# Kernel optimization log

Measured on AMD Instinct MI355X. Metric: run time of the kernel, lower is better.

## Reference

```python
import jax, jax.numpy as jnp
import numpy as np

NCA_HIDDEN = 16
N_CODES = 32
EMBED_DIM = 64


def conv2d(x, w, pad, b=None):
    # x: (N, Cin, H, W), w: (Cout, Cin, kh, kw)
    y = jax.lax.conv_general_dilated(
        x, w, window_strides=(1, 1), padding=[(pad, pad), (pad, pad)],
        dimension_numbers=('NCHW', 'OIHW', 'NCHW'))
    if b is not None:
        y = y + b[None, :, None, None]
    return y


def setup_inputs() -> dict:
    key = jax.random.key(0)
    ks = jax.random.split(key, 32)
    rn = lambda k, shp, s=0.05: jax.random.normal(k, shp, dtype=jnp.float32) * s
    H = NCA_HIDDEN
    upd = H * H * 3 * 3  # 2304
    tau = H * H          # 256
    inp = {
        'demo_inputs':  jax.random.normal(ks[0], (8, 1, 64, 64), dtype=jnp.float32),
        'demo_outputs': jax.random.normal(ks[1], (8, 1, 64, 64), dtype=jnp.float32),
        'test_input':   jax.random.normal(ks[2], (16, 1, 256, 256), dtype=jnp.float32),
        # TaskEncoder params
        'enc_w1': rn(ks[3], (16, 2, 3, 3)),  'enc_b1': jnp.zeros((16,), jnp.float32),
        'enc_w2': rn(ks[4], (32, 16, 3, 3)), 'enc_b2': jnp.zeros((32,), jnp.float32),
        'enc_lw': rn(ks[5], (EMBED_DIM, 32)), 'enc_lb': jnp.zeros((EMBED_DIM,), jnp.float32),
        # gen_update hypernet
        'gu_w1': rn(ks[6], (128, EMBED_DIM)), 'gu_b1': jnp.zeros((128,), jnp.float32),
        'gu_w2': rn(ks[7], (upd, 128)),       'gu_b2': jnp.zeros((upd,), jnp.float32),
        # gen_tau hypernet
        'gt_w1': rn(ks[8], (64, EMBED_DIM)),  'gt_b1': jnp.zeros((64,), jnp.float32),
        'gt_w2': rn(ks[9], (tau, 64)),        'gt_b2': jnp.zeros((tau,), jnp.float32),
        # stem
        'stem_w': rn(ks[10], (H, 1, 3, 3)), 'stem_b': jnp.zeros((H,), jnp.float32),
        # VQ codebook, init U(-1/n_codes, 1/n_codes)
        'codebook': jax.random.uniform(ks[11], (N_CODES, H), jnp.float32,
                                       minval=-1.0 / N_CODES, maxval=1.0 / N_CODES),
        # decoder 1x1 conv
        'dec_w': rn(ks[12], (1, H, 1, 1)), 'dec_b': jnp.zeros((1,), jnp.float32),
        'n_steps': 5,
    }
    return inp


def reference(demo_inputs, demo_outputs, test_input,
              enc_w1, enc_b1, enc_w2, enc_b2, enc_lw, enc_lb,
              gu_w1, gu_b1, gu_w2, gu_b2,
              gt_w1, gt_b1, gt_w2, gt_b2,
              stem_w, stem_b, codebook, dec_w, dec_b, n_steps):
    H = NCA_HIDDEN
    # --- Task encoder: mean task embedding over demo pairs ---
    pairs = jnp.concatenate([demo_inputs, demo_outputs], axis=1)  # (N,2,h,w)
    h = jax.nn.relu(conv2d(pairs, enc_w1, 1, enc_b1))
    h = jax.nn.relu(conv2d(h, enc_w2, 1, enc_b2))
    h = h.mean(axis=(2, 3))                   # AdaptiveAvgPool2d(1)+Flatten -> (N,32)
    te = (h @ enc_lw.T + enc_lb).mean(axis=0)  # (embed_dim,)
    # --- Hypernetworks generate NCA weights ---
    W_update = (jax.nn.relu(te @ gu_w1.T + gu_b1) @ gu_w2.T + gu_b2).reshape(H, H, 3, 3)
    W_tau = (jax.nn.relu(te @ gt_w1.T + gt_b1) @ gt_w2.T + gt_b2).reshape(H, H, 1, 1)
    # --- Stem ---
    state = jax.nn.relu(conv2d(test_input, stem_w, 1, stem_b))  # (B,16,Hh,Ww)
    cb_sq = (codebook ** 2).sum(axis=1)  # (n_codes,)
    for _ in range(int(n_steps)):
        delta = jax.nn.relu(conv2d(state, W_update, 1))
        beta = jax.nn.sigmoid(conv2d(state, W_tau, 0))
        state = beta * state + (1.0 - beta) * delta
        # --- VQ step (straight-through) ---
        B, C, Hh, Ww = state.shape
        zf = state.transpose(0, 2, 3, 1).reshape(-1, C)  # (B*Hh*Ww, C)
        dists = (zf ** 2).sum(1, keepdims=True) + cb_sq - 2.0 * (zf @ codebook.T)
        idx = jnp.argmin(dists, axis=1)
        zq = codebook[idx].reshape(B, Hh, Ww, C).transpose(0, 3, 1, 2)
        state = state + jax.lax.stop_gradient(zq - state)
    output = jax.nn.sigmoid(conv2d(state, dec_w, 0, dec_b))
    return output
```

## Files before the change

kernel.cpp:

```cpp
#include <hip/hip_runtime.h>
#include <stdint.h>

#define NPIX 65536
#define NIMG 16

typedef float4 F4;
typedef _Float16 h2v __attribute__((ext_vector_type(2)));
typedef _Float16 h8v __attribute__((ext_vector_type(8)));
typedef float    f4v __attribute__((ext_vector_type(4)));

union H8 { h8v v; h2v p[4]; _Float16 e[8]; };

__device__ __forceinline__ float sigm(float x){ return 1.0f/(1.0f+__expf(-x)); }

#if defined(__has_builtin)
#if __has_builtin(__builtin_amdgcn_rcpf)
#define FRCP(x) __builtin_amdgcn_rcpf(x)
#endif
#endif
#ifndef FRCP
#define FRCP(x) (1.0f/(x))
#endif
__device__ __forceinline__ float sigmf(float x){ return FRCP(1.0f + __expf(-x)); }

__device__ __forceinline__ h2v pkrtz(float a, float b){
  return __builtin_bit_cast(h2v, __builtin_amdgcn_cvt_pkrtz(a,b));
}

#if defined(__has_builtin)
#if __has_builtin(__builtin_amdgcn_fdot2)
#define FDOT2(a,b,c) __builtin_amdgcn_fdot2((a),(b),(c),false)
#endif
#endif
#ifndef FDOT2
#define FDOT2(a,b,c) ((c) + (float)(a)[0]*(float)(b)[0] + (float)(a)[1]*(float)(b)[1])
#endif

__global__ __launch_bounds__(256) void k_enc1(
    const float* __restrict__ din, const float* __restrict__ dou,
    const float* __restrict__ w1, const float* __restrict__ b1,
    float* __restrict__ h1)
{
  int n = blockIdx.x;
  int p = blockIdx.y*256 + threadIdx.x;
  int y = p >> 6, x = p & 63;
  const float* in0 = din + n*4096;
  const float* in1 = dou + n*4096;
  float acc[16];
  #pragma unroll
  for(int c=0;c<16;c++) acc[c]=b1[c];
  for(int ky=0;ky<3;ky++){
    int yy=y+ky-1; if((unsigned)yy>=64u) continue;
    for(int kx=0;kx<3;kx++){
      int xx=x+kx-1; if((unsigned)xx>=64u) continue;
      float v0=in0[yy*64+xx], v1=in1[yy*64+xx];
      #pragma unroll
      for(int co=0;co<16;co++)
        acc[co] += w1[co*18+ky*3+kx]*v0 + w1[co*18+9+ky*3+kx]*v1;
    }
  }
  F4* o=(F4*)(h1 + (size_t)(n*4096+p)*16);
  o[0]=make_float4(fmaxf(acc[0],0.f),fmaxf(acc[1],0.f),fmaxf(acc[2],0.f),fmaxf(acc[3],0.f));
  o[1]=make_float4(fmaxf(acc[4],0.f),fmaxf(acc[5],0.f),fmaxf(acc[6],0.f),fmaxf(acc[7],0.f));
  o[2]=make_float4(fmaxf(acc[8],0.f),fmaxf(acc[9],0.f),fmaxf(acc[10],0.f),fmaxf(acc[11],0.f));
  o[3]=make_float4(fmaxf(acc[12],0.f),fmaxf(acc[13],0.f),fmaxf(acc[14],0.f),fmaxf(acc[15],0.f));
}

__global__ __launch_bounds__(256) void k_enc2(
    const float* __restrict__ h1, const float* __restrict__ w2,
    const float* __restrict__ b2, float* __restrict__ pooled)
{
  int n = blockIdx.x;
  int p = blockIdx.y*256 + threadIdx.x;
  int y = p >> 6, x = p & 63;
  float acc[32];
  #pragma unroll
  for(int c=0;c<32;c++) acc[c]=b2[c];
  for(int ky=0;ky<3;ky++){
    int yy=y+ky-1; if((unsigned)yy>=64u) continue;
    for(int kx=0;kx<3;kx++){
      int xx=x+kx-1; if((unsigned)xx>=64u) continue;
      const F4* hp=(const F4*)(h1 + (size_t)(n*4096 + yy*64+xx)*16);
      F4 a0=hp[0],a1=hp[1],a2=hp[2],a3=hp[3];
      float hv[16]={a0.x,a0.y,a0.z,a0.w,a1.x,a1.y,a1.z,a1.w,
                    a2.x,a2.y,a2.z,a2.w,a3.x,a3.y,a3.z,a3.w};
      #pragma unroll
      for(int ci=0;ci<16;ci++){
        float v=hv[ci];
        #pragma unroll
        for(int co=0;co<32;co++)
          acc[co] = fmaf(w2[co*144 + ci*9 + ky*3+kx], v, acc[co]);
      }
    }
  }
  #pragma unroll
  for(int c=0;c<32;c++) acc[c]=fmaxf(acc[c],0.f);
  __shared__ float red[4][32];
  int lane = threadIdx.x & 63, wv = threadIdx.x >> 6;
  #pragma unroll
  for(int c=0;c<32;c++){
    float v=acc[c];
    for(int off=32;off>=1;off>>=1) v += __shfl_down(v, off, 64);
    if(lane==0) red[wv][c]=v;
  }
  __syncthreads();
  if(threadIdx.x<32){
    float s = red[0][threadIdx.x]+red[1][threadIdx.x]+red[2][threadIdx.x]+red[3][threadIdx.x];
    atomicAdd(&pooled[n*32+threadIdx.x], s);
  }
}

__global__ __launch_bounds__(256) void k_hyperA(
    const float* __restrict__ pooled,
    const float* __restrict__ lw, const float* __restrict__ lb,
    const float* __restrict__ guw1, const float* __restrict__ gub1,
    const float* __restrict__ gtw1, const float* __restrict__ gtb1,
    const float* __restrict__ gtw2, const float* __restrict__ gtb2,
    const float* __restrict__ cb, const float* __restrict__ decw, const float* __restrict__ decb,
    float* __restrict__ hid_g,
    _Float16* __restrict__ wfrag_g,
    _Float16* __restrict__ Mh_g,
    _Float16* __restrict__ bcb_g, _Float16* __restrict__ omb_g,
    _Float16* __restrict__ cbh_g,
    float* __restrict__ chs_g, float* __restrict__ dvals_g)
{
  __shared__ float hm[32], te_s[64], hid_s[128], hidt_s[64];
  __shared__ float wt_s[256];
  __shared__ float cb_s[512];
  int t = threadIdx.x;
  for(int i=t;i<2560;i+=256) ((unsigned int*)wfrag_g)[i]=0u;
  for(int i=t;i<2508;i+=256) ((unsigned int*)Mh_g)[i]=0u;
  if(t<32){
    float s=0.f;
    for(int n=0;n<8;n++) s += pooled[n*32+t];
    hm[t] = s * (1.0f/32768.0f);
  }
  for(int i=t;i<512;i+=256) cb_s[i]=cb[i];
  __syncthreads();
  if(t<64){
    float s=lb[t];
    for(int c=0;c<32;c++) s = fmaf(lw[t*32+c], hm[c], s);
    te_s[t]=s;
  }
  __syncthreads();
  if(t<128){
    float s=gub1[t];
    for(int j=0;j<64;j++) s = fmaf(guw1[t*64+j], te_s[j], s);
    s=fmaxf(s,0.f);
    hid_s[t]=s; hid_g[t]=s;
  } else if(t<192){
    int i=t-128;
    float s=gtb1[i];
    for(int j=0;j<64;j++) s = fmaf(gtw1[i*64+j], te_s[j], s);
    hidt_s[i]=fmaxf(s,0.f);
  }
  __syncthreads();
  {
    float s=gtb2[t];
    for(int i=0;i<64;i++) s = fmaf(gtw2[t*64+i], hidt_s[i], s);
    int co=t>>4, ci=t&15;
    wt_s[ci*16+co]=s;
  }
  __syncthreads();
  {
    int ci=t>>4, co=t&15;
    int g=ci>>3, j=ci&7, lane=(g<<4)|co;
    wfrag_g[(448+lane)*8+j]=(_Float16)wt_s[ci*16+co];
  }
  for(int o=t;o<512;o+=256){
    int k=o>>4, c=o&15;
    float T=0.f;
    for(int ci=0;ci<16;ci++) T = fmaf(wt_s[ci*16+c], cb_s[k*16+ci], T);
    float beta=sigm(T);
    bcb_g[o]=(_Float16)(beta*cb_s[o]);
    omb_g[o]=(_Float16)(1.f-beta);
    cbh_g[o]=(_Float16)cb_s[o];
  }
  if(t<32){
    float sq=0.f, d=0.f;
    for(int c=0;c<16;c++){ float v=cb_s[t*16+c]; sq=fmaf(v,v,sq); d=fmaf(decw[c],v,d); }
    chs_g[t]=0.5f*sq;
    dvals_g[t]=sigm(d+decb[0]);
  }
}

__global__ __launch_bounds__(256) void k_hyperB(
    const float* __restrict__ guw2, const float* __restrict__ gub2,
    const float* __restrict__ hid_g, const float* __restrict__ cb,
    _Float16* __restrict__ wfrag_g, _Float16* __restrict__ Mh_g)
{
  __shared__ float hid_s[128];
  __shared__ float wu_s[256];
  __shared__ float cb_s[512];
  const int t=threadIdx.x, tp=blockIdx.x;
  if(t<128) hid_s[t]=hid_g[t];
  for(int i=t;i<512;i+=256) cb_s[i]=cb[i];
  __syncthreads();
  const int ci=t>>4, co=t&15;
  const int o=co*144+ci*9+tp;
  float s=gub2[o];
  const F4* gp=(const F4*)(guw2+(size_t)o*128);
  #pragma unroll
  for(int i=0;i<32;i++){
    F4 g=gp[i];
    s=fmaf(g.x,hid_s[4*i],s); s=fmaf(g.y,hid_s[4*i+1],s);
    s=fmaf(g.z,hid_s[4*i+2],s); s=fmaf(g.w,hid_s[4*i+3],s);
  }
  wu_s[ci*16+co]=s;
  {
    int k=tp*16+ci;
    int ks=k>>5, rem=k&31, g2=rem>>3, j=rem&7, lane=(g2<<4)|co;
    wfrag_g[(ks*64+lane)*8+j]=(_Float16)s;
  }
  __syncthreads();
  for(int o2=t;o2<512;o2+=256){
    int k=o2>>4, c=o2&15;
    float m=0.f;
    for(int c2=0;c2<16;c2++) m=fmaf(wu_s[c2*16+c], cb_s[k*16+c2], m);
    Mh_g[k*152+tp*16+c]=(_Float16)m;
  }
}

#define ST_STRIDE 3
struct S1P1 { h8v st[324*ST_STRIDE]; float in[400]; };
union S1U { S1P1 p; unsigned int dt[256*20]; };

__global__ __launch_bounds__(256) void k_step1(
    const float* __restrict__ tin,
    const float* __restrict__ stw, const float* __restrict__ stb,
    const _Float16* __restrict__ wfrag,
    const _Float16* __restrict__ cbh, const float* __restrict__ chs,
    uint8_t* __restrict__ idx_out)
{
  __shared__ S1U u;
  __shared__ h8v cb8_s[64];
  __shared__ float chs_s[32];
  __shared__ h2v stwp_s[72];
  __shared__ h2v stbp_s[8];

  const int tid=threadIdx.x;
  const int bx=blockIdx.x, by=blockIdx.y, n=blockIdx.z;
  const float* in = tin + (size_t)n*NPIX;

  for(int i=tid;i<400;i+=256){
    int sy=i/20, sx=i-sy*20;
    int gy=by*16-2+sy, gx=bx*16-2+sx;
    u.p.in[i] = ((unsigned)gy<256u && (unsigned)gx<256u) ? in[gy*256+gx] : 0.0f;
  }
  if(tid<72){
    int q=tid/9, tp=tid-q*9;
    stwp_s[q*9+tp]=pkrtz(stw[(2*q)*9+tp], stw[(2*q+1)*9+tp]);
  } else if(tid<80){
    int q=tid-72;
    stbp_s[q]=pkrtz(stb[2*q], stb[2*q+1]);
  } else if(tid>=160 && tid<192) chs_s[tid-160]=chs[tid-160];
  if(tid<64) ((uint4*)cb8_s)[tid] = ((const uint4*)cbh)[tid];

  const int lane = tid & 63, w = tid >> 6;
  const int g = lane >> 4, nn = lane & 15;
  h8v Bd[5], Bt2;
  const h8v* wf = (const h8v*)wfrag;
  #pragma unroll
  for(int ks=0;ks<5;ks++) Bd[ks]=wf[ks*64+lane];
  Bt2 = wf[7*64+lane];

  __syncthreads();

  for(int p=tid;p<324;p+=256){
    int syh=p/18, sxh=p-syh*18;
    int gy=by*16-1+syh, gx=bx*16-1+sxh;
    H8 b0,b1;
    if((unsigned)gy<256u && (unsigned)gx<256u){
      h2v a2[8];
      #pragma unroll
      for(int q=0;q<8;q++) a2[q]=stbp_s[q];
      #pragma unroll
      for(int ky=0;ky<3;ky++){
        #pragma unroll
        for(int kx=0;kx<3;kx++){
          int tp=ky*3+kx;
          float v=u.p.in[(syh+ky)*20+(sxh+kx)];
          h2v vv=pkrtz(v,v);
          #pragma unroll
          for(int q=0;q<8;q++) a2[q] = stwp_s[q*9+tp]*vv + a2[q];
        }
      }
      b0.p[0]=a2[0]; b0.p[1]=a2[1]; b0.p[2]=a2[2]; b0.p[3]=a2[3];
      b1.p[0]=a2[4]; b1.p[1]=a2[5]; b1.p[2]=a2[6]; b1.p[3]=a2[7];
      #pragma unroll
      for(int c=0;c<8;c++){
        b0.e[c]=b0.e[c]>(_Float16)0?b0.e[c]:(_Float16)0;
        b1.e[c]=b1.e[c]>(_Float16)0?b1.e[c]:(_Float16)0;
      }
    } else {
      b0.v=(h8v){0,0,0,0,0,0,0,0};
      b1.v=(h8v){0,0,0,0,0,0,0,0};
    }
    u.p.st[p*ST_STRIDE]  =b0.v;
    u.p.st[p*ST_STRIDE+1]=b1.v;
  }
  __syncthreads();

  f4v accd[4], acct[4];
  #pragma unroll
  for(int m=0;m<4;m++){ accd[m]=(f4v){0.f,0.f,0.f,0.f}; acct[m]=(f4v){0.f,0.f,0.f,0.f}; }
  #pragma unroll
  for(int ks=0;ks<5;ks++){
    int t = 2*ks + (g>>1); if(t>8) t=8;
    int tyo=(t*11)>>5, txo=t-tyo*3;
    int sel = g&1;
    #pragma unroll
    for(int m=0;m<4;m++){
      int sy = 4*w+m+tyo;
      h8v a = u.p.st[(sy*18 + nn + txo)*ST_STRIDE + sel];
      accd[m]=__builtin_amdgcn_mfma_f32_16x16x32_f16(a,Bd[ks],accd[m],0,0,0);
      if(ks==2) acct[m]=__builtin_amdgcn_mfma_f32_16x16x32_f16(a,Bt2,acct[m],0,0,0);
    }
  }
  const int py=tid>>4, pxx=tid&15;
  const int cpx=((py+1)*18+pxx+1)*ST_STRIDE;
  h8v z0=u.p.st[cpx], z1=u.p.st[cpx+1];
  __syncthreads();

  #pragma unroll
  for(int m=0;m<4;m++){
    #pragma unroll
    for(int r=0;r<4;r++){
      int px=(4*w+m)*16 + g*4 + r;
      h2v pk = pkrtz(accd[m][r], acct[m][r]);
      u.dt[px*20+nn] = __builtin_bit_cast(unsigned int, pk);
    }
  }
  __syncthreads();

  const uint4* dr=(const uint4*)(u.dt+tid*20);
  uint4 q0=dr[0],q1=dr[1],q2=dr[2],q3=dr[3];
  unsigned int qq[16]={q0.x,q0.y,q0.z,q0.w,q1.x,q1.y,q1.z,q1.w,
                       q2.x,q2.y,q2.z,q2.w,q3.x,q3.y,q3.z,q3.w};
  float zn[16];
  #pragma unroll
  for(int c=0;c<16;c++){
    h2v dt2=__builtin_bit_cast(h2v, qq[c]);
    float d=(float)dt2[0]; d = d>0.f?d:0.f;
    float beta=sigmf((float)dt2[1]);
    float zv = (c<8)? (float)z0[c] : (float)z1[c-8];
    zn[c]=fmaf(beta, zv-d, d);
  }
  H8 u0,u1;
  #pragma unroll
  for(int j=0;j<4;j++){
    u0.p[j]=pkrtz(zn[2*j],zn[2*j+1]);
    u1.p[j]=pkrtz(zn[8+2*j],zn[9+2*j]);
  }
  int best=0; float bv=-3.4e38f;
  #pragma unroll
  for(int k=0;k<32;k++){
    H8 c0,c1; c0.v=cb8_s[k*2]; c1.v=cb8_s[k*2+1];
    float dot=0.f;
    #pragma unroll
    for(int j=0;j<4;j++) dot=FDOT2(u0.p[j],c0.p[j],dot);
    #pragma unroll
    for(int j=0;j<4;j++) dot=FDOT2(u1.p[j],c1.p[j],dot);
    float val=dot-chs_s[k];
    if(val>bv){bv=val;best=k;}
  }
  idx_out[(size_t)n*NPIX + (by*16+py)*256 + (bx*16+pxx)]=(uint8_t)best;
}

__global__ __launch_bounds__(256) void k_stepN(
    const uint8_t* __restrict__ idx_in,
    const uint4* __restrict__ Mh,
    const _Float16* __restrict__ bcbh, const _Float16* __restrict__ ombh,
    const _Float16* __restrict__ cbh,  const float* __restrict__ chs,
    const float* __restrict__ dvals,
    uint8_t* __restrict__ idx_out, float* __restrict__ out, int last)
{
  __shared__ int id_s[324];
  __shared__ uint4 M_s[627];
  __shared__ h8v bcb_s[64], omb_s[64], cb8_s[64];
  __shared__ float chs_s[32], dv_s[32];
  const int tid=threadIdx.x;
  const int bx=blockIdx.x, by=blockIdx.y, n=blockIdx.z;
  const uint8_t* ip = idx_in + (size_t)n*NPIX;

  for(int i=tid;i<324;i+=256){
    int sy=i/18, sx=i-sy*18;
    int gy=by*16-1+sy, gx=bx*16-1+sx;
    id_s[i] = ((unsigned)gy<256u && (unsigned)gx<256u) ? (int)ip[gy*256+gx] : 32;
  }
  for(int i=tid;i<627;i+=256) M_s[i]=Mh[i];
  if(tid<64)        ((uint4*)bcb_s)[tid]     = ((const uint4*)bcbh)[tid];
  else if(tid<128)  ((uint4*)omb_s)[tid-64]  = ((const uint4*)ombh)[tid-64];
  else if(tid<192)  ((uint4*)cb8_s)[tid-128] = ((const uint4*)cbh)[tid-128];
  else if(tid<224)  chs_s[tid-192]=chs[tid-192];
  else              dv_s[tid-224]=dvals[tid-224];
  __syncthreads();

  const int py=tid>>4, pxx=tid&15;
  int ida[9];
  #pragma unroll
  for(int dy=0;dy<3;dy++)
    #pragma unroll
    for(int dx=0;dx<3;dx++)
      ida[dy*3+dx]=id_s[(py+dy)*18+pxx+dx];

  const h8v* Mv=(const h8v*)M_s;
  h8v a0={0,0,0,0,0,0,0,0}, a1={0,0,0,0,0,0,0,0};
  #pragma unroll
  for(int t=0;t<9;t++){
    const h8v* mp=&Mv[ida[t]*19+t*2];
    a0+=mp[0]; a1+=mp[1];
  }
  int kc=ida[4];
  h8v r0,r1;
  #pragma unroll
  for(int q=0;q<8;q++){
    r0[q]=a0[q]>(_Float16)0?a0[q]:(_Float16)0;
    r1[q]=a1[q]>(_Float16)0?a1[q]:(_Float16)0;
  }
  H8 u0,u1;
  u0.v = bcb_s[kc*2]   + omb_s[kc*2]  *r0;
  u1.v = bcb_s[kc*2+1] + omb_s[kc*2+1]*r1;
  int best=0; float bv=-3.4e38f;
  #pragma unroll
  for(int k=0;k<32;k++){
    H8 c0,c1; c0.v=cb8_s[k*2]; c1.v=cb8_s[k*2+1];
    float dot=0.f;
    #pragma unroll
    for(int j=0;j<4;j++) dot=FDOT2(u0.p[j],c0.p[j],dot);
    #pragma unroll
    for(int j=0;j<4;j++) dot=FDOT2(u1.p[j],c1.p[j],dot);
    float val=dot-chs_s[k];
    if(val>bv){bv=val;best=k;}
  }
  size_t gidx=(size_t)n*NPIX + (size_t)(by*16+py)*256 + bx*16+pxx;
  if(last) out[gidx]=dv_s[best];
  else     idx_out[gidx]=(uint8_t)best;
}

extern "C" void kernel_launch(void* const* d_in, const int* in_sizes, int n_in,
                              void* d_out, int out_size, void* d_ws, size_t ws_size,
                              hipStream_t stream)
{
  const float* demo_in  = (const float*)d_in[0];
  const float* demo_out = (const float*)d_in[1];
  const float* test_in  = (const float*)d_in[2];
  const float* enc_w1 = (const float*)d_in[3];
  const float* enc_b1 = (const float*)d_in[4];
  const float* enc_w2 = (const float*)d_in[5];
  const float* enc_b2 = (const float*)d_in[6];
  const float* enc_lw = (const float*)d_in[7];
  const float* enc_lb = (const float*)d_in[8];
  const float* gu_w1 = (const float*)d_in[9];
  const float* gu_b1 = (const float*)d_in[10];
  const float* gu_w2 = (const float*)d_in[11];
  const float* gu_b2 = (const float*)d_in[12];
  const float* gt_w1 = (const float*)d_in[13];
  const float* gt_b1 = (const float*)d_in[14];
  const float* gt_w2 = (const float*)d_in[15];
  const float* gt_b2 = (const float*)d_in[16];
  const float* stem_w = (const float*)d_in[17];
  const float* stem_b = (const float*)d_in[18];
  const float* codebook = (const float*)d_in[19];
  const float* dec_w = (const float*)d_in[20];
  const float* dec_b = (const float*)d_in[21];

  float* ws = (float*)d_ws;
  float* h1     = ws;
  float* pooled = h1 + 524288;
  float* chs    = pooled + 256;
  float* dvals  = chs + 32;
  float* hid_g  = dvals + 32;
  _Float16* hbase = (_Float16*)(ws + 524736);
  _Float16* wfrag = hbase;
  _Float16* Mh    = hbase + 5120;
  _Float16* bcbh  = hbase + 10144;
  _Float16* ombh  = hbase + 10656;
  _Float16* cbh   = hbase + 11168;
  uint8_t* idxA = (uint8_t*)(hbase + 11680);
  uint8_t* idxB = idxA + (size_t)NIMG*NPIX;

  (void)hipMemsetAsync(pooled, 0, 256*sizeof(float), stream);
  k_enc1<<<dim3(8,16),256,0,stream>>>(demo_in, demo_out, enc_w1, enc_b1, h1);
  k_enc2<<<dim3(8,16),256,0,stream>>>(h1, enc_w2, enc_b2, pooled);
  k_hyperA<<<1,256,0,stream>>>(pooled, enc_lw, enc_lb,
                               gu_w1,gu_b1, gt_w1,gt_b1, gt_w2,gt_b2,
                               codebook, dec_w, dec_b,
                               hid_g, wfrag, Mh, bcbh, ombh, cbh, chs, dvals);
  k_hyperB<<<9,256,0,stream>>>(gu_w2, gu_b2, hid_g, codebook, wfrag, Mh);
  dim3 tgrid(16,16,NIMG);
  k_step1<<<tgrid,256,0,stream>>>(test_in, stem_w, stem_b, wfrag, cbh, chs, idxA);
  float* outp = (float*)d_out;
  k_stepN<<<tgrid,256,0,stream>>>(idxA,(const uint4*)Mh,bcbh,ombh,cbh,chs,dvals, idxB,outp,0);
  k_stepN<<<tgrid,256,0,stream>>>(idxB,(const uint4*)Mh,bcbh,ombh,cbh,chs,dvals, idxA,outp,0);
  k_stepN<<<tgrid,256,0,stream>>>(idxA,(const uint4*)Mh,bcbh,ombh,cbh,chs,dvals, idxB,outp,0);
  k_stepN<<<tgrid,256,0,stream>>>(idxB,(const uint4*)Mh,bcbh,ombh,cbh,chs,dvals, idxA,outp,1);
}
```

Baseline: 287.5 us.

## Fuse encoder convs with MFMA and fuse four NCA steps with halo recompute

Replaces the two encoder kernels with a single tiled kernel that computes conv1 into shared memory in fp16 and runs conv2 with 16x16x32 MFMA instructions, using weights pre-packed by a new prep kernel. The h1 round trip through global memory goes away. The four separate code-index step kernels become one kernel that keeps a 40x40 index tile in shared memory and runs four steps with a shrinking halo. This trades three launches and the global index traffic for redundant halo recompute and larger shared-memory use. The encoder now carries fp16 rounding in conv1 activations and conv2.

```diff
diff --git a/kernel.cpp b/kernel.cpp
--- a/kernel.cpp
+++ b/kernel.cpp
@@ -36,77 +36,132 @@
 #define FDOT2(a,b,c) ((c) + (float)(a)[0]*(float)(b)[0] + (float)(a)[1]*(float)(b)[1])
 #endif
 
-__global__ __launch_bounds__(256) void k_enc1(
+__global__ __launch_bounds__(256) void k_prep(
+    const float* __restrict__ w2, _Float16* __restrict__ wfragE)
+{
+  int t=threadIdx.x;
+  for(int i=t;i<5120;i+=256){
+    int j=i&7, rest=i>>3, lane=rest&63, rest2=rest>>6, ks=rest2%5, b=rest2/5;
+    int g=lane>>4, nn=lane&15;
+    int k=32*ks+8*g+j;
+    float v=0.f;
+    if(k<144){
+      int tap=2*ks+(g>>1), ci=8*(g&1)+j, co=b*16+nn;
+      v=w2[co*144+ci*9+tap];
+    }
+    wfragE[i]=(_Float16)v;
+  }
+}
+
+__global__ __launch_bounds__(256) void k_enc(
     const float* __restrict__ din, const float* __restrict__ dou,
     const float* __restrict__ w1, const float* __restrict__ b1,
-    float* __restrict__ h1)
-{
-  int n = blockIdx.x;
-  int p = blockIdx.y*256 + threadIdx.x;
-  int y = p >> 6, x = p & 63;
-  const float* in0 = din + n*4096;
-  const float* in1 = dou + n*4096;
-  float acc[16];
-  #pragma unroll
-  for(int c=0;c<16;c++) acc[c]=b1[c];
-  for(int ky=0;ky<3;ky++){
-    int yy=y+ky-1; if((unsigned)yy>=64u) continue;
-    for(int kx=0;kx<3;kx++){
-      int xx=x+kx-1; if((unsigned)xx>=64u) continue;
-      float v0=in0[yy*64+xx], v1=in1[yy*64+xx];
-      #pragma unroll
-      for(int co=0;co<16;co++)
-        acc[co] += w1[co*18+ky*3+kx]*v0 + w1[co*18+9+ky*3+kx]*v1;
-    }
-  }
-  F4* o=(F4*)(h1 + (size_t)(n*4096+p)*16);
-  o[0]=make_float4(fmaxf(acc[0],0.f),fmaxf(acc[1],0.f),fmaxf(acc[2],0.f),fmaxf(acc[3],0.f));
-  o[1]=make_float4(fmaxf(acc[4],0.f),fmaxf(acc[5],0.f),fmaxf(acc[6],0.f),fmaxf(acc[7],0.f));
-  o[2]=make_float4(fmaxf(acc[8],0.f),fmaxf(acc[9],0.f),fmaxf(acc[10],0.f),fmaxf(acc[11],0.f));
-  o[3]=make_float4(fmaxf(acc[12],0.f),fmaxf(acc[13],0.f),fmaxf(acc[14],0.f),fmaxf(acc[15],0.f));
-}
-
-__global__ __launch_bounds__(256) void k_enc2(
-    const float* __restrict__ h1, const float* __restrict__ w2,
-    const float* __restrict__ b2, float* __restrict__ pooled)
-{
-  int n = blockIdx.x;
-  int p = blockIdx.y*256 + threadIdx.x;
-  int y = p >> 6, x = p & 63;
-  float acc[32];
-  #pragma unroll
-  for(int c=0;c<32;c++) acc[c]=b2[c];
-  for(int ky=0;ky<3;ky++){
-    int yy=y+ky-1; if((unsigned)yy>=64u) continue;
-    for(int kx=0;kx<3;kx++){
-      int xx=x+kx-1; if((unsigned)xx>=64u) continue;
-      const F4* hp=(const F4*)(h1 + (size_t)(n*4096 + yy*64+xx)*16);
-      F4 a0=hp[0],a1=hp[1],a2=hp[2],a3=hp[3];
-      float hv[16]={a0.x,a0.y,a0.z,a0.w,a1.x,a1.y,a1.z,a1.w,
-                    a2.x,a2.y,a2.z,a2.w,a3.x,a3.y,a3.z,a3.w};
-      #pragma unroll
-      for(int ci=0;ci<16;ci++){
-        float v=hv[ci];
+    const float* __restrict__ b2,
+    const _Float16* __restrict__ wfragE,
+    float* __restrict__ pooled)
+{
+  __shared__ float2 in_s[400];
+  __shared__ h8v st_h[324*3];
+  __shared__ float red[4][32];
+  __shared__ h2v stwp_s[144];
+  __shared__ h2v stbp_s[8];
+
+  const int tid=threadIdx.x;
+  const int bx=blockIdx.x, by=blockIdx.y, n=blockIdx.z;
+  const float* i0 = din + n*4096;
+  const float* i1 = dou + n*4096;
+
+  for(int i=tid;i<400;i+=256){
+    int sy=i/20, sx=i-sy*20;
+    int gy=by*16-2+sy, gx=bx*16-2+sx;
+    bool ok=((unsigned)gy<64u && (unsigned)gx<64u);
+    in_s[i] = ok ? make_float2(i0[gy*64+gx], i1[gy*64+gx]) : make_float2(0.f,0.f);
+  }
+  if(tid<144){
+    int q=tid/18, r=tid-18*q;
+    stwp_s[tid]=pkrtz(w1[36*q+r], w1[36*q+18+r]);
+  } else if(tid<152){
+    int q=tid-144;
+    stbp_s[q]=pkrtz(b1[2*q], b1[2*q+1]);
+  }
+
+  const int lane=tid&63, w=tid>>6, g=lane>>4, nn=lane&15;
+  h8v B0[5], B1[5];
+  const h8v* wfE=(const h8v*)wfragE;
+  #pragma unroll
+  for(int ks=0;ks<5;ks++){ B0[ks]=wfE[ks*64+lane]; B1[ks]=wfE[(5+ks)*64+lane]; }
+  float b2a=b2[nn], b2b=b2[nn+16];
+  __syncthreads();
+
+  for(int p=tid;p<324;p+=256){
+    int syh=p/18, sxh=p-syh*18;
+    int gy=by*16-1+syh, gx=bx*16-1+sxh;
+    H8 o0,o1;
+    if((unsigned)gy<64u && (unsigned)gx<64u){
+      h2v a2[8];
+      #pragma unroll
+      for(int q=0;q<8;q++) a2[q]=stbp_s[q];
+      #pragma unroll
+      for(int ky=0;ky<3;ky++){
         #pragma unroll
-        for(int co=0;co<32;co++)
-          acc[co] = fmaf(w2[co*144 + ci*9 + ky*3+kx], v, acc[co]);
+        for(int kx=0;kx<3;kx++){
+          int tp=ky*3+kx;
+          float2 v=in_s[(syh+ky)*20+(sxh+kx)];
+          h2v v0=pkrtz(v.x,v.x), v1=pkrtz(v.y,v.y);
+          #pragma unroll
+          for(int q=0;q<8;q++){
+            a2[q]=stwp_s[(2*q)*9+tp]*v0 + a2[q];
+            a2[q]=stwp_s[(2*q+1)*9+tp]*v1 + a2[q];
+          }
+        }
       }
-    }
-  }
-  #pragma unroll
-  for(int c=0;c<32;c++) acc[c]=fmaxf(acc[c],0.f);
-  __shared__ float red[4][32];
-  int lane = threadIdx.x & 63, wv = threadIdx.x >> 6;
-  #pragma unroll
-  for(int c=0;c<32;c++){
-    float v=acc[c];
-    for(int off=32;off>=1;off>>=1) v += __shfl_down(v, off, 64);
-    if(lane==0) red[wv][c]=v;
-  }
-  __syncthreads();
-  if(threadIdx.x<32){
-    float s = red[0][threadIdx.x]+red[1][threadIdx.x]+red[2][threadIdx.x]+red[3][threadIdx.x];
-    atomicAdd(&pooled[n*32+threadIdx.x], s);
+      o0.p[0]=a2[0]; o0.p[1]=a2[1]; o0.p[2]=a2[2]; o0.p[3]=a2[3];
+      o1.p[0]=a2[4]; o1.p[1]=a2[5]; o1.p[2]=a2[6]; o1.p[3]=a2[7];
+      #pragma unroll
+      for(int c=0;c<8;c++){
+        o0.e[c]=o0.e[c]>(_Float16)0?o0.e[c]:(_Float16)0;
+        o1.e[c]=o1.e[c]>(_Float16)0?o1.e[c]:(_Float16)0;
+      }
+    } else {
+      o0.v=(h8v){0,0,0,0,0,0,0,0};
+      o1.v=(h8v){0,0,0,0,0,0,0,0};
+    }
+    st_h[p*3]  =o0.v;
+    st_h[p*3+1]=o1.v;
+  }
+  __syncthreads();
+
+  f4v acc0[4], acc1[4];
+  #pragma unroll
+  for(int m=0;m<4;m++){ acc0[m]=(f4v){0.f,0.f,0.f,0.f}; acc1[m]=(f4v){0.f,0.f,0.f,0.f}; }
+  #pragma unroll
+  for(int ks=0;ks<5;ks++){
+    int t=2*ks+(g>>1); if(t>8) t=8;
+    int tyo=(t*11)>>5, txo=t-tyo*3;
+    int sel=g&1;
+    #pragma unroll
+    for(int m=0;m<4;m++){
+      int sy=4*w+m+tyo;
+      h8v a=st_h[(sy*18+nn+txo)*3+sel];
+      acc0[m]=__builtin_amdgcn_mfma_f32_16x16x32_f16(a,B0[ks],acc0[m],0,0,0);
+      acc1[m]=__builtin_amdgcn_mfma_f32_16x16x32_f16(a,B1[ks],acc1[m],0,0,0);
+    }
+  }
+  float s0=0.f, s1=0.f;
+  #pragma unroll
+  for(int m=0;m<4;m++)
+    #pragma unroll
+    for(int r=0;r<4;r++){
+      s0+=fmaxf(acc0[m][r]+b2a,0.f);
+      s1+=fmaxf(acc1[m][r]+b2b,0.f);
+    }
+  s0+=__shfl_down(s0,32,64); s0+=__shfl_down(s0,16,64);
+  s1+=__shfl_down(s1,32,64); s1+=__shfl_down(s1,16,64);
+  if(lane<16){ red[w][nn]=s0; red[w][nn+16]=s1; }
+  __syncthreads();
+  if(tid<32){
+    float s=red[0][tid]+red[1][tid]+red[2][tid]+red[3][tid];
+    atomicAdd(&pooled[n*32+tid], s);
   }
 }
 
@@ -367,26 +422,85 @@
   idx_out[(size_t)n*NPIX + (by*16+py)*256 + (bx*16+pxx)]=(uint8_t)best;
 }
 
-__global__ __launch_bounds__(256) void k_stepN(
+__device__ __forceinline__ void nca_step(
+    const int* __restrict__ src, int* __restrict__ dst,
+    int w, int lo, int gy0, int gx0, int n,
+    const h8v* Mv, const h8v* bcb_s, const h8v* omb_s, const h8v* cb8_s,
+    const float* chs_s, const float* dv_s,
+    float* __restrict__ out, bool last, int tid)
+{
+  const int count=w*w;
+  for(int it=0; it<6; it++){
+    int c = tid + it*256;
+    if(c>=count) break;
+    int ry=c/w, rx=c-ry*w;
+    int sy=lo+ry, sx=lo+rx;
+    int base=(sy-1)*40+sx-1;
+    int i0=src[base],    i1=src[base+1],  i2=src[base+2];
+    int i3=src[base+40], i4=src[base+41], i5=src[base+42];
+    int i6=src[base+80], i7=src[base+81], i8=src[base+82];
+    h8v a0={0,0,0,0,0,0,0,0}, a1={0,0,0,0,0,0,0,0};
+    { const h8v* mp=&Mv[i0*19+0];  a0+=mp[0]; a1+=mp[1]; }
+    { const h8v* mp=&Mv[i1*19+2];  a0+=mp[0]; a1+=mp[1]; }
+    { const h8v* mp=&Mv[i2*19+4];  a0+=mp[0]; a1+=mp[1]; }
+    { const h8v* mp=&Mv[i3*19+6];  a0+=mp[0]; a1+=mp[1]; }
+    { const h8v* mp=&Mv[i4*19+8];  a0+=mp[0]; a1+=mp[1]; }
+    { const h8v* mp=&Mv[i5*19+10]; a0+=mp[0]; a1+=mp[1]; }
+    { const h8v* mp=&Mv[i6*19+12]; a0+=mp[0]; a1+=mp[1]; }
+    { const h8v* mp=&Mv[i7*19+14]; a0+=mp[0]; a1+=mp[1]; }
+    { const h8v* mp=&Mv[i8*19+16]; a0+=mp[0]; a1+=mp[1]; }
+    h8v r0,r1;
+    #pragma unroll
+    for(int q=0;q<8;q++){
+      r0[q]=a0[q]>(_Float16)0?a0[q]:(_Float16)0;
+      r1[q]=a1[q]>(_Float16)0?a1[q]:(_Float16)0;
+    }
+    H8 u0,u1;
+    u0.v = bcb_s[i4*2]   + omb_s[i4*2]  *r0;
+    u1.v = bcb_s[i4*2+1] + omb_s[i4*2+1]*r1;
+    int best=0; float bv=-3.4e38f;
+    #pragma unroll
+    for(int k=0;k<32;k++){
+      H8 c0,c1; c0.v=cb8_s[k*2]; c1.v=cb8_s[k*2+1];
+      float dot=0.f;
+      #pragma unroll
+      for(int j=0;j<4;j++) dot=FDOT2(u0.p[j],c0.p[j],dot);
+      #pragma unroll
+      for(int j=0;j<4;j++) dot=FDOT2(u1.p[j],c1.p[j],dot);
+      float val=dot-chs_s[k];
+      if(val>bv){bv=val;best=k;}
+    }
+    if(last){
+      out[(size_t)n*NPIX + (size_t)(gy0+sy)*256 + (gx0+sx)] = dv_s[best];
+    } else {
+      int gy=gy0+sy, gx=gx0+sx;
+      bool in=((unsigned)gy<256u && (unsigned)gx<256u);
+      dst[sy*40+sx] = in ? best : 32;
+    }
+  }
+}
+
+__global__ __launch_bounds__(256) void k_step4(
     const uint8_t* __restrict__ idx_in,
     const uint4* __restrict__ Mh,
     const _Float16* __restrict__ bcbh, const _Float16* __restrict__ ombh,
     const _Float16* __restrict__ cbh,  const float* __restrict__ chs,
     const float* __restrict__ dvals,
-    uint8_t* __restrict__ idx_out, float* __restrict__ out, int last)
-{
-  __shared__ int id_s[324];
+    float* __restrict__ out)
+{
+  __shared__ int idA[1600], idB[1600];
   __shared__ uint4 M_s[627];
   __shared__ h8v bcb_s[64], omb_s[64], cb8_s[64];
   __shared__ float chs_s[32], dv_s[32];
   const int tid=threadIdx.x;
   const int bx=blockIdx.x, by=blockIdx.y, n=blockIdx.z;
   const uint8_t* ip = idx_in + (size_t)n*NPIX;
-
-  for(int i=tid;i<324;i+=256){
-    int sy=i/18, sx=i-sy*18;
-    int gy=by*16-1+sy, gx=bx*16-1+sx;
-    id_s[i] = ((unsigned)gy<256u && (unsigned)gx<256u) ? (int)ip[gy*256+gx] : 32;
+  const int gy0=by*32-4, gx0=bx*32-4;
+
+  for(int i=tid;i<1600;i+=256){
+    int sy=i/40, sx=i-sy*40;
+    int gy=gy0+sy, gx=gx0+sx;
+    idA[i] = ((unsigned)gy<256u && (unsigned)gx<256u) ? (int)ip[gy*256+gx] : 32;
   }
   for(int i=tid;i<627;i+=256) M_s[i]=Mh[i];
   if(tid<64)        ((uint4*)bcb_s)[tid]     = ((const uint4*)bcbh)[tid];
@@ -396,46 +510,14 @@
   else              dv_s[tid-224]=dvals[tid-224];
   __syncthreads();
 
-  const int py=tid>>4, pxx=tid&15;
-  int ida[9];
-  #pragma unroll
-  for(int dy=0;dy<3;dy++)
-    #pragma unroll
-    for(int dx=0;dx<3;dx++)
-      ida[dy*3+dx]=id_s[(py+dy)*18+pxx+dx];
-
   const h8v* Mv=(const h8v*)M_s;
-  h8v a0={0,0,0,0,0,0,0,0}, a1={0,0,0,0,0,0,0,0};
-  #pragma unroll
-  for(int t=0;t<9;t++){
-    const h8v* mp=&Mv[ida[t]*19+t*2];
-    a0+=mp[0]; a1+=mp[1];
-  }
-  int kc=ida[4];
-  h8v r0,r1;
-  #pragma unroll
-  for(int q=0;q<8;q++){
-    r0[q]=a0[q]>(_Float16)0?a0[q]:(_Float16)0;
-    r1[q]=a1[q]>(_Float16)0?a1[q]:(_Float16)0;
-  }
-  H8 u0,u1;
-  u0.v = bcb_s[kc*2]   + omb_s[kc*2]  *r0;
-  u1.v = bcb_s[kc*2+1] + omb_s[kc*2+1]*r1;
-  int best=0; float bv=-3.4e38f;
-  #pragma unroll
-  for(int k=0;k<32;k++){
-    H8 c0,c1; c0.v=cb8_s[k*2]; c1.v=cb8_s[k*2+1];
-    float dot=0.f;
-    #pragma unroll
-    for(int j=0;j<4;j++) dot=FDOT2(u0.p[j],c0.p[j],dot);
-    #pragma unroll
-    for(int j=0;j<4;j++) dot=FDOT2(u1.p[j],c1.p[j],dot);
-    float val=dot-chs_s[k];
-    if(val>bv){bv=val;best=k;}
-  }
-  size_t gidx=(size_t)n*NPIX + (size_t)(by*16+py)*256 + bx*16+pxx;
-  if(last) out[gidx]=dv_s[best];
-  else     idx_out[gidx]=(uint8_t)best;
+  nca_step(idA,idB,38,1,gy0,gx0,n,Mv,bcb_s,omb_s,cb8_s,chs_s,dv_s,out,false,tid);
+  __syncthreads();
+  nca_step(idB,idA,36,2,gy0,gx0,n,Mv,bcb_s,omb_s,cb8_s,chs_s,dv_s,out,false,tid);
+  __syncthreads();
+  nca_step(idA,idB,34,3,gy0,gx0,n,Mv,bcb_s,omb_s,cb8_s,chs_s,dv_s,out,false,tid);
+  __syncthreads();
+  nca_step(idB,nullptr,32,4,gy0,gx0,n,Mv,bcb_s,omb_s,cb8_s,chs_s,dv_s,out,true,tid);
 }
 
 extern "C" void kernel_launch(void* const* d_in, const int* in_sizes, int n_in,
@@ -466,23 +548,22 @@
   const float* dec_b = (const float*)d_in[21];
 
   float* ws = (float*)d_ws;
-  float* h1     = ws;
-  float* pooled = h1 + 524288;
+  float* pooled = ws;
   float* chs    = pooled + 256;
   float* dvals  = chs + 32;
   float* hid_g  = dvals + 32;
-  _Float16* hbase = (_Float16*)(ws + 524736);
-  _Float16* wfrag = hbase;
-  _Float16* Mh    = hbase + 5120;
-  _Float16* bcbh  = hbase + 10144;
-  _Float16* ombh  = hbase + 10656;
-  _Float16* cbh   = hbase + 11168;
-  uint8_t* idxA = (uint8_t*)(hbase + 11680);
-  uint8_t* idxB = idxA + (size_t)NIMG*NPIX;
+  _Float16* hbase = (_Float16*)(ws + 448);
+  _Float16* wfrag  = hbase;
+  _Float16* wfragE = hbase + 5120;
+  _Float16* Mh     = hbase + 10240;
+  _Float16* bcbh   = hbase + 15264;
+  _Float16* ombh   = hbase + 15776;
+  _Float16* cbh    = hbase + 16288;
+  uint8_t* idxA = (uint8_t*)(hbase + 16800);
 
   (void)hipMemsetAsync(pooled, 0, 256*sizeof(float), stream);
-  k_enc1<<<dim3(8,16),256,0,stream>>>(demo_in, demo_out, enc_w1, enc_b1, h1);
-  k_enc2<<<dim3(8,16),256,0,stream>>>(h1, enc_w2, enc_b2, pooled);
+  k_prep<<<1,256,0,stream>>>(enc_w2, wfragE);
+  k_enc<<<dim3(4,4,8),256,0,stream>>>(demo_in, demo_out, enc_w1, enc_b1, enc_b2, wfragE, pooled);
   k_hyperA<<<1,256,0,stream>>>(pooled, enc_lw, enc_lb,
                                gu_w1,gu_b1, gt_w1,gt_b1, gt_w2,gt_b2,
                                codebook, dec_w, dec_b,
@@ -491,8 +572,5 @@
   dim3 tgrid(16,16,NIMG);
   k_step1<<<tgrid,256,0,stream>>>(test_in, stem_w, stem_b, wfrag, cbh, chs, idxA);
   float* outp = (float*)d_out;
-  k_stepN<<<tgrid,256,0,stream>>>(idxA,(const uint4*)Mh,bcbh,ombh,cbh,chs,dvals, idxB,outp,0);
-  k_stepN<<<tgrid,256,0,stream>>>(idxB,(const uint4*)Mh,bcbh,ombh,cbh,chs,dvals, idxA,outp,0);
-  k_stepN<<<tgrid,256,0,stream>>>(idxA,(const uint4*)Mh,bcbh,ombh,cbh,chs,dvals, idxB,outp,0);
-  k_stepN<<<tgrid,256,0,stream>>>(idxB,(const uint4*)Mh,bcbh,ombh,cbh,chs,dvals, idxA,outp,1);
-}
+  k_step4<<<dim3(8,8,NIMG),256,0,stream>>>(idxA,(const uint4*)Mh,bcbh,ombh,cbh,chs,dvals, outp);
+}
```

Measured after the change: 347.3 us. 20.8% more time.
